# Performance work log

Measured on AMD Instinct MI355X. Metric: run time of the kernel, lower is better.

The kernel has to match this reference:

```python
import jax, jax.numpy as jnp
import numpy as np


def setup_inputs() -> dict:
    key = jax.random.key(0)
    k1, k2 = jax.random.split(key)
    B, K, S = 262144, 32, 30
    sparse_code = jax.random.normal(k1, (B, K), dtype=jnp.float32)
    dictionary = jax.random.normal(k2, (S * S, K), dtype=jnp.float32)
    return {"sparse_code": sparse_code, "dictionary": dictionary, "image_size": S}


def reference(sparse_code, dictionary, image_size):
    # matmul(dictionary, sparse_code.T).T == sparse_code @ dictionary.T -> [B, S*S]
    samples = jnp.einsum("bk,dk->bd", sparse_code, dictionary)
    B = samples.shape[0]
    img = samples.reshape(B, image_size, image_size)
    # Serpentine unrolling: flip every odd row (rows 1,3,...,image_size-1)
    img = img.at[:, 1::2, :].set(img[:, 1::2, ::-1])
    return img[:, None, :, :]  # [B, 1, S, S]
```

## Files before the change

### kernel.cpp

```cpp
#include <hip/hip_runtime.h>
#include <hip/hip_bf16.h>


typedef __attribute__((ext_vector_type(8))) short bf16x8;
typedef __attribute__((ext_vector_type(4))) float f32x4;

constexpr int KD    = 32;
constexpr int DDIM  = 900;
constexpr int SDIM  = 30;
constexpr int NCHT  = 57;
constexpr int TROWS = 16;
constexpr int TILES = 16;
constexpr int RPB   = TROWS * TILES;
constexpr int TFL   = TROWS * DDIM;

__device__ __forceinline__ int serp_src(int d) {
    int r = d / SDIM, c = d - r * SDIM;
    return (r & 1) ? (r * SDIM + (SDIM - 1 - c)) : d;
}

__device__ __forceinline__ short f2bf(float x) {
    __hip_bfloat16 h = __float2bfloat16(x);
    short u; __builtin_memcpy(&u, &h, 2); return u;
}

__device__ __forceinline__ void barrier_lds() {
    __builtin_amdgcn_sched_barrier(0);
    asm volatile("s_waitcnt lgkmcnt(0)" ::: "memory");
    __builtin_amdgcn_sched_barrier(0);
    __builtin_amdgcn_s_barrier();
    __builtin_amdgcn_sched_barrier(0);
}

__global__ __launch_bounds__(512, 1) void mfma_decode(
    const float* __restrict__ sc,
    const float* __restrict__ dict,
    float* __restrict__ out,
    int B)
{
    __shared__ alignas(16) float stg[2][TFL];

    const int t    = threadIdx.x;
    const int lane = t & 63;
    const int wid  = t >> 6;

    const int brow = lane & 15;
    const int k0   = (lane >> 4) << 3;
    const int dloc = (lane >> 4) << 2;
    const long long b0 = (long long)blockIdx.x * RPB;

    bf16x8 df[15];
    bf16x8 bb[TILES];

    auto compute = [&](const bf16x8& bbx, float* buf) {
        #pragma unroll
        for (int j = 0; j < 15; ++j) {
            const int ch = wid + 4 * j;
            if (ch < NCHT) {
                f32x4 z = {0.f, 0.f, 0.f, 0.f};
                f32x4 acc = __builtin_amdgcn_mfma_f32_16x16x32_bf16(df[j], bbx, z, 0, 0, 0);
                if (ch != 56) {
                    *reinterpret_cast<f32x4*>(&buf[brow * DDIM + ch * 16 + dloc]) = acc;
                } else if (dloc == 0) {
                    *reinterpret_cast<f32x4*>(&buf[brow * DDIM + 896]) = acc;
                }
            }
        }
    };

    if (wid < 4) {
        #pragma unroll
        for (int j = 0; j < 15; ++j) {
            int ch = wid + 4 * j; if (ch > NCHT - 1) ch = NCHT - 1;
            int d  = ch * 16 + (lane & 15);
            int dd = (d < DDIM) ? d : (DDIM - 1);
            const float* p = dict + (size_t)serp_src(dd) * KD + k0;
            const float4 f0 = *reinterpret_cast<const float4*>(p);
            const float4 f1 = *reinterpret_cast<const float4*>(p + 4);
            bf16x8 a;
            a[0] = f2bf(f0.x); a[1] = f2bf(f0.y); a[2] = f2bf(f0.z); a[3] = f2bf(f0.w);
            a[4] = f2bf(f1.x); a[5] = f2bf(f1.y); a[6] = f2bf(f1.z); a[7] = f2bf(f1.w);
            df[j] = a;
        }

        #pragma unroll
        for (int g = 0; g < TILES / 4; ++g) {
            float4 ra[4], rb[4];
            #pragma unroll
            for (int u = 0; u < 4; ++u) {
                const int tt = g * 4 + u;
                const float* ap = sc + (size_t)(b0 + tt * TROWS + brow) * KD + k0;
                ra[u] = *reinterpret_cast<const float4*>(ap);
                rb[u] = *reinterpret_cast<const float4*>(ap + 4);
            }
            #pragma unroll
            for (int u = 0; u < 4; ++u) {
                bf16x8 r;
                r[0] = f2bf(ra[u].x); r[1] = f2bf(ra[u].y);
                r[2] = f2bf(ra[u].z); r[3] = f2bf(ra[u].w);
                r[4] = f2bf(rb[u].x); r[5] = f2bf(rb[u].y);
                r[6] = f2bf(rb[u].z); r[7] = f2bf(rb[u].w);
                bb[g * 4 + u] = r;
            }
        }

        compute(bb[0], stg[0]);
    }
    barrier_lds();

    const int base = (t - 256) * 4;

    #pragma unroll
    for (int tile = 0; tile < TILES; ++tile) {
        if (wid < 4) {
            if (tile + 1 < TILES) compute(bb[tile + 1], stg[(tile + 1) & 1]);
        } else {
            const float* __restrict__ buf = stg[tile & 1];
            float* __restrict__ tbase =
                out + (size_t)(b0 + (long long)tile * TROWS) * DDIM;
            #pragma unroll
            for (int i = 0; i < 14; ++i) {
                const int o = i * 1024 + base;
                f32x4 v = *reinterpret_cast<const f32x4*>(&buf[o]);
                *reinterpret_cast<f32x4*>(tbase + o) = v;
            }
            if (t < 272) {
                const int o = 14336 + base;
                f32x4 v = *reinterpret_cast<const f32x4*>(&buf[o]);
                *reinterpret_cast<f32x4*>(tbase + o) = v;
            }
        }
        barrier_lds();
    }
}

extern "C" void kernel_launch(void* const* d_in, const int* in_sizes, int n_in,
                              void* d_out, int out_size, void* d_ws, size_t ws_size,
                              hipStream_t stream) {
    const float* sc   = (const float*)d_in[0];
    const float* dict = (const float*)d_in[1];
    float* out        = (float*)d_out;

    const int B = in_sizes[0] / KD;

    mfma_decode<<<dim3((unsigned)(B / RPB)), 512, 0, stream>>>(sc, dict, out, B);
}
```

Before: 195.1 us.

## Drop producer/consumer wave split and process more tiles per block

The kernel drops the split into 4 MFMA-producer waves and 4 store waves. It now runs 256-thread blocks where every wave computes one tile into LDS and then copies the previous tile to global memory. Each block handles 64 tiles instead of 16, so the grid shrinks to about one block per CU. Input rows are prefetched a group ahead into registers to hide load latency. This cuts launch and block-scheduling overhead and the tail effect, but stores and MFMA work now run serially within each wave instead of overlapping across specialised waves. The kernel is already near the output-bandwidth limit.

```diff
diff --git a/kernel.cpp b/kernel.cpp
--- a/kernel.cpp
+++ b/kernel.cpp
@@ -10,7 +10,9 @@
 constexpr int SDIM  = 30;
 constexpr int NCHT  = 57;
 constexpr int TROWS = 16;
-constexpr int TILES = 16;
+constexpr int GROUP = 8;
+constexpr int NGRP  = 8;
+constexpr int TILES = GROUP * NGRP;
 constexpr int RPB   = TROWS * TILES;
 constexpr int TFL   = TROWS * DDIM;
 
@@ -32,7 +34,7 @@
     __builtin_amdgcn_sched_barrier(0);
 }
 
-__global__ __launch_bounds__(512, 1) void mfma_decode(
+__global__ __launch_bounds__(256, 1) void mfma_decode(
     const float* __restrict__ sc,
     const float* __restrict__ dict,
     float* __restrict__ out,
@@ -50,7 +52,43 @@
     const long long b0 = (long long)blockIdx.x * RPB;
 
     bf16x8 df[15];
-    bf16x8 bb[TILES];
+    #pragma unroll
+    for (int j = 0; j < 15; ++j) {
+        int ch = wid + 4 * j; if (ch > NCHT - 1) ch = NCHT - 1;
+        int d  = ch * 16 + (lane & 15);
+        int dd = (d < DDIM) ? d : (DDIM - 1);
+        const float* p = dict + (size_t)serp_src(dd) * KD + k0;
+        const float4 f0 = *reinterpret_cast<const float4*>(p);
+        const float4 f1 = *reinterpret_cast<const float4*>(p + 4);
+        bf16x8 a;
+        a[0] = f2bf(f0.x); a[1] = f2bf(f0.y); a[2] = f2bf(f0.z); a[3] = f2bf(f0.w);
+        a[4] = f2bf(f1.x); a[5] = f2bf(f1.y); a[6] = f2bf(f1.z); a[7] = f2bf(f1.w);
+        df[j] = a;
+    }
+
+    float4 ra[GROUP], rb[GROUP];
+    auto load_group = [&](int g) {
+        #pragma unroll
+        for (int u = 0; u < GROUP; ++u) {
+            const long long tt = (long long)g * GROUP + u;
+            const float* ap = sc + (size_t)(b0 + tt * TROWS + brow) * KD + k0;
+            ra[u] = *reinterpret_cast<const float4*>(ap);
+            rb[u] = *reinterpret_cast<const float4*>(ap + 4);
+        }
+    };
+
+    bf16x8 bb[GROUP];
+    auto cvt_group = [&]() {
+        #pragma unroll
+        for (int u = 0; u < GROUP; ++u) {
+            bf16x8 r;
+            r[0] = f2bf(ra[u].x); r[1] = f2bf(ra[u].y);
+            r[2] = f2bf(ra[u].z); r[3] = f2bf(ra[u].w);
+            r[4] = f2bf(rb[u].x); r[5] = f2bf(rb[u].y);
+            r[6] = f2bf(rb[u].z); r[7] = f2bf(rb[u].w);
+            bb[u] = r;
+        }
+    };
 
     auto compute = [&](const bf16x8& bbx, float* buf) {
         #pragma unroll
@@ -68,69 +106,43 @@
         }
     };
 
-    if (wid < 4) {
-        #pragma unroll
-        for (int j = 0; j < 15; ++j) {
-            int ch = wid + 4 * j; if (ch > NCHT - 1) ch = NCHT - 1;
-            int d  = ch * 16 + (lane & 15);
-            int dd = (d < DDIM) ? d : (DDIM - 1);
-            const float* p = dict + (size_t)serp_src(dd) * KD + k0;
-            const float4 f0 = *reinterpret_cast<const float4*>(p);
-            const float4 f1 = *reinterpret_cast<const float4*>(p + 4);
-            bf16x8 a;
-            a[0] = f2bf(f0.x); a[1] = f2bf(f0.y); a[2] = f2bf(f0.z); a[3] = f2bf(f0.w);
-            a[4] = f2bf(f1.x); a[5] = f2bf(f1.y); a[6] = f2bf(f1.z); a[7] = f2bf(f1.w);
-            df[j] = a;
-        }
-
-        #pragma unroll
-        for (int g = 0; g < TILES / 4; ++g) {
-            float4 ra[4], rb[4];
-            #pragma unroll
-            for (int u = 0; u < 4; ++u) {
-                const int tt = g * 4 + u;
-                const float* ap = sc + (size_t)(b0 + tt * TROWS + brow) * KD + k0;
-                ra[u] = *reinterpret_cast<const float4*>(ap);
-                rb[u] = *reinterpret_cast<const float4*>(ap + 4);
-            }
-            #pragma unroll
-            for (int u = 0; u < 4; ++u) {
-                bf16x8 r;
-                r[0] = f2bf(ra[u].x); r[1] = f2bf(ra[u].y);
-                r[2] = f2bf(ra[u].z); r[3] = f2bf(ra[u].w);
-                r[4] = f2bf(rb[u].x); r[5] = f2bf(rb[u].y);
-                r[6] = f2bf(rb[u].z); r[7] = f2bf(rb[u].w);
-                bb[g * 4 + u] = r;
-            }
-        }
-
-        compute(bb[0], stg[0]);
-    }
+    load_group(0);
+    cvt_group();
+    compute(bb[0], stg[0]);
     barrier_lds();
 
-    const int base = (t - 256) * 4;
+    const int base = t * 4;
 
-    #pragma unroll
-    for (int tile = 0; tile < TILES; ++tile) {
-        if (wid < 4) {
-            if (tile + 1 < TILES) compute(bb[tile + 1], stg[(tile + 1) & 1]);
-        } else {
-            const float* __restrict__ buf = stg[tile & 1];
-            float* __restrict__ tbase =
-                out + (size_t)(b0 + (long long)tile * TROWS) * DDIM;
+    for (int g = 0; g < NGRP; ++g) {
+        #pragma unroll
+        for (int u = 0; u < GROUP; ++u) {
+            const long long tile = (long long)g * GROUP + u;
+
+            if (u == GROUP - 2 && g + 1 < NGRP) load_group(g + 1);
+
+            if (u < GROUP - 1) {
+                compute(bb[u + 1], stg[(u + 1) & 1]);
+            } else if (g + 1 < NGRP) {
+                cvt_group();
+                compute(bb[0], stg[(u + 1) & 1]);
+            }
+
+            float* __restrict__ tbase = out + (size_t)(b0 + tile * TROWS) * DDIM;
+            const float* __restrict__ buf = stg[u & 1];
             #pragma unroll
             for (int i = 0; i < 14; ++i) {
                 const int o = i * 1024 + base;
                 f32x4 v = *reinterpret_cast<const f32x4*>(&buf[o]);
                 *reinterpret_cast<f32x4*>(tbase + o) = v;
             }
-            if (t < 272) {
+            if (t < 16) {
                 const int o = 14336 + base;
                 f32x4 v = *reinterpret_cast<const f32x4*>(&buf[o]);
                 *reinterpret_cast<f32x4*>(tbase + o) = v;
             }
+
+            barrier_lds();
         }
-        barrier_lds();
     }
 }
 
@@ -143,5 +155,5 @@
 
     const int B = in_sizes[0] / KD;
 
-    mfma_decode<<<dim3((unsigned)(B / RPB)), 512, 0, stream>>>(sc, dict, out, B);
+    mfma_decode<<<dim3((unsigned)(B / RPB)), 256, 0, stream>>>(sc, dict, out, B);
 }
```

After: 202.7 us. +3.9%, slower.
